# Optimization experiments

Measured on AMD Instinct MI355X. Metric: run time of the kernel, lower is better.

The kernel has to match this reference:

```python
import jax, jax.numpy as jnp
import numpy as np

ALPHA = 1.5
N_ITER = 5
N_SECTIONS = 5


def setup_inputs() -> dict:
    key = jax.random.key(0)
    X = jax.random.normal(key, (4096, 32000), dtype=jnp.float32)
    return {"X": X}


def reference(X) -> jnp.ndarray:
    # entmax_nsect: find tau such that sum_j [(alpha-1)*X_j - tau]_+^{1/(alpha-1)} = 1
    # via n-section search (n_iter rounds, interval split into n_sections).
    alpha = ALPHA
    Xs = X * (alpha - 1.0)                      # work in transformed logits
    d = X.shape[-1]
    exp_inv = 1.0 / (alpha - 1.0)

    max_val = jnp.max(Xs, axis=-1, keepdims=True)
    lo = max_val - 1.0                          # f(lo) >= 0
    hi = max_val - (1.0 / d) ** (alpha - 1.0)   # f(hi) <= 0

    def f(tau):
        # sum of p(tau) minus 1; monotonically decreasing in tau
        p = jnp.clip(Xs - tau, 0.0, None) ** exp_inv
        return jnp.sum(p, axis=-1, keepdims=True) - 1.0

    for _ in range(N_ITER):
        width = (hi - lo) / N_SECTIONS
        new_lo = lo
        # pick the largest interior grid point where f is still >= 0
        for k in range(1, N_SECTIONS):
            t = lo + k * width
            new_lo = jnp.where(f(t) >= 0.0, t, new_lo)
        lo = new_lo
        hi = new_lo + width

    tau = 0.5 * (lo + hi)
    p = jnp.clip(Xs - tau, 0.0, None) ** exp_inv
    # ensure_sum_one=True
    p = p / jnp.sum(p, axis=-1, keepdims=True)
    return p
```

## Files before the change

### kernel.cpp

```cpp
#include <hip/hip_runtime.h>
#include <math.h>

#define D_DIM 32000
#define NV4   8000
#define BLOCK 256
#define KMAX  32
#define NBINS 256

#define BINW_F   3.8844134767822285e-3f
#define INVBW_F  257.43893f

typedef float floatx4 __attribute__((ext_vector_type(4)));


__global__ void __launch_bounds__(BLOCK, 3)
entmax_nsect_kernel(const float* __restrict__ X, float* __restrict__ out, int n_rows) {
    const int row = blockIdx.x;
    if (row >= n_rows) return;
    const int tid  = threadIdx.x;
    const int lane = tid & 63;
    const int wid  = tid >> 6;

    __shared__ __align__(16) float sC[NBINS];
    __shared__ __align__(16) float sS[NBINS];
    __shared__ __align__(16) float sQ[NBINS];
    __shared__ float s_wmax[4];

    const float4* __restrict__ xrow = reinterpret_cast<const float4*>(X + (size_t)row * D_DIM);
    floatx4* __restrict__ orow      = reinterpret_cast<floatx4*>(out + (size_t)row * D_DIM);

    float4 v[KMAX];
#pragma unroll
    for (int k = 0; k < KMAX; ++k) {
        const int j = tid + k * BLOCK;
        if (j < NV4) v[k] = xrow[j];
        else         v[k] = make_float4(-INFINITY, -INFINITY, -INFINITY, -INFINITY);
    }
#pragma unroll
    for (int k = 0; k < KMAX; ++k)
        asm volatile("" : "+v"(v[k].x), "+v"(v[k].y), "+v"(v[k].z), "+v"(v[k].w));

    sC[tid] = 0.0f; sS[tid] = 0.0f; sQ[tid] = 0.0f;

    float mx = -INFINITY;
#pragma unroll
    for (int k = 0; k < KMAX; ++k)
        mx = fmaxf(mx, fmaxf(fmaxf(v[k].x, v[k].y), fmaxf(v[k].z, v[k].w)));
#pragma unroll
    for (int o = 32; o > 0; o >>= 1) mx = fmaxf(mx, __shfl_xor(mx, o));
    if (lane == 0) s_wmax[wid] = mx;
    __syncthreads();

    const float m0 = fmaxf(fmaxf(s_wmax[0], s_wmax[1]), fmaxf(s_wmax[2], s_wmax[3]));
    const float maxXs = 0.5f * m0;

#pragma unroll
    for (int k = 0; k < KMAX; ++k) {
        const float ys[4] = { fmaf(v[k].x, 0.5f, -maxXs),
                              fmaf(v[k].y, 0.5f, -maxXs),
                              fmaf(v[k].z, 0.5f, -maxXs),
                              fmaf(v[k].w, 0.5f, -maxXs) };
#pragma unroll
        for (int c = 0; c < 4; ++c) {
            const float y = ys[c];
            if (y > -1.0f) {
                const int b = (int)fminf((y + 1.0f) * INVBW_F, 255.0f);
                atomicAdd(&sC[b], 1.0f);
                atomicAdd(&sS[b], y);
                atomicAdd(&sQ[b], y * y);
            }
        }
    }
    __syncthreads();

    if (wid < 3) {
        float* plane = (wid == 0) ? sC : (wid == 1) ? sS : sQ;
        const float4 f = reinterpret_cast<const float4*>(plane)[lane];
        const float t3 = f.w;
        const float t2 = f.z + t3;
        const float t1 = f.y + t2;
        const float t0 = f.x + t1;
        float inc = t0;
#pragma unroll
        for (int o = 1; o < 64; o <<= 1) {
            const float u = __shfl_down(inc, o);
            if (lane + o < 64) inc += u;
        }
        const float above = inc - t0;
        float4 o4;
        o4.x = t0 + above; o4.y = t1 + above; o4.z = t2 + above; o4.w = t3 + above;
        reinterpret_cast<float4*>(plane)[lane] = o4;
    }
    __syncthreads();

    int klo = 0, khi = 256;
#pragma unroll
    for (int it = 0; it < 8; ++it) {
        const int mid = (klo + khi) >> 1;
        const float t  = fmaf((float)mid, BINW_F, -1.0f);
        const float fm = fmaf(t, fmaf(t, sC[mid], -2.0f * sS[mid]), sQ[mid]);
        if (fm >= 1.0f) klo = mid; else khi = mid;
    }
    const float C = sC[klo], S = sS[klo], Q = sQ[klo];
    const float disc = fmaxf(fmaf(S, S, -C * (Q - 1.0f)), 0.0f);
    float tauY = (S - sqrtf(disc)) / C;
    tauY = fminf(fmaxf(tauY, -1.0f), 0.0f);
    const float tau = maxXs + tauY;

#pragma unroll
    for (int k = 0; k < KMAX; ++k) {
        const int j = tid + k * BLOCK;
        if (j < NV4) {
            float d;
            floatx4 p;
            d = fmaxf(fmaf(v[k].x, 0.5f, -tau), 0.f); p.x = d * d;
            d = fmaxf(fmaf(v[k].y, 0.5f, -tau), 0.f); p.y = d * d;
            d = fmaxf(fmaf(v[k].z, 0.5f, -tau), 0.f); p.z = d * d;
            d = fmaxf(fmaf(v[k].w, 0.5f, -tau), 0.f); p.w = d * d;
            __builtin_nontemporal_store(p, &orow[j]);
        }
    }
}

extern "C" void kernel_launch(void* const* d_in, const int* in_sizes, int n_in,
                              void* d_out, int out_size, void* d_ws, size_t ws_size,
                              hipStream_t stream) {
    const float* X = (const float*)d_in[0];
    float* out     = (float*)d_out;
    const int n_rows = in_sizes[0] / D_DIM;
    entmax_nsect_kernel<<<dim3(n_rows), dim3(BLOCK), 0, stream>>>(X, out, n_rows);
}
```

Baseline: 204.4 us.

## Stream row from memory three times instead of caching it in registers

Drops the 32-float4 register cache of each row and re-reads the row from global memory in the max, histogram and output passes. The launch bound rises from 3 to 8 blocks per SIMD, so more waves can be resident to hide latency. Each row is 128KB, so re-reads are meant to hit L2 or the infinity cache. The trade-off is roughly three times more load traffic through the cache hierarchy, and a DRAM-bound slowdown if those re-reads miss.

```diff
diff --git a/kernel.cpp b/kernel.cpp
--- a/kernel.cpp
+++ b/kernel.cpp
@@ -4,7 +4,7 @@
 #define D_DIM 32000
 #define NV4   8000
 #define BLOCK 256
-#define KMAX  32
+#define KFULL 31
 #define NBINS 256
 
 #define BINW_F   3.8844134767822285e-3f
@@ -13,7 +13,7 @@
 typedef float floatx4 __attribute__((ext_vector_type(4)));
 
 
-__global__ void __launch_bounds__(BLOCK, 3)
+__global__ void __launch_bounds__(BLOCK, 8)
 entmax_nsect_kernel(const float* __restrict__ X, float* __restrict__ out, int n_rows) {
     const int row = blockIdx.x;
     if (row >= n_rows) return;
@@ -29,23 +29,18 @@
     const float4* __restrict__ xrow = reinterpret_cast<const float4*>(X + (size_t)row * D_DIM);
     floatx4* __restrict__ orow      = reinterpret_cast<floatx4*>(out + (size_t)row * D_DIM);
 
-    float4 v[KMAX];
-#pragma unroll
-    for (int k = 0; k < KMAX; ++k) {
-        const int j = tid + k * BLOCK;
-        if (j < NV4) v[k] = xrow[j];
-        else         v[k] = make_float4(-INFINITY, -INFINITY, -INFINITY, -INFINITY);
-    }
-#pragma unroll
-    for (int k = 0; k < KMAX; ++k)
-        asm volatile("" : "+v"(v[k].x), "+v"(v[k].y), "+v"(v[k].z), "+v"(v[k].w));
-
     sC[tid] = 0.0f; sS[tid] = 0.0f; sQ[tid] = 0.0f;
 
     float mx = -INFINITY;
-#pragma unroll
-    for (int k = 0; k < KMAX; ++k)
-        mx = fmaxf(mx, fmaxf(fmaxf(v[k].x, v[k].y), fmaxf(v[k].z, v[k].w)));
+#pragma unroll 4
+    for (int k = 0; k < KFULL; ++k) {
+        const float4 a = xrow[tid + k * BLOCK];
+        mx = fmaxf(mx, fmaxf(fmaxf(a.x, a.y), fmaxf(a.z, a.w)));
+    }
+    if (tid < 64) {
+        const float4 a = xrow[tid + KFULL * BLOCK];
+        mx = fmaxf(mx, fmaxf(fmaxf(a.x, a.y), fmaxf(a.z, a.w)));
+    }
 #pragma unroll
     for (int o = 32; o > 0; o >>= 1) mx = fmaxf(mx, __shfl_xor(mx, o));
     if (lane == 0) s_wmax[wid] = mx;
@@ -54,12 +49,26 @@
     const float m0 = fmaxf(fmaxf(s_wmax[0], s_wmax[1]), fmaxf(s_wmax[2], s_wmax[3]));
     const float maxXs = 0.5f * m0;
 
+#pragma unroll 4
+    for (int k = 0; k < KFULL; ++k) {
+        const float4 a = xrow[tid + k * BLOCK];
+        const float ys[4] = { fmaf(a.x, 0.5f, -maxXs), fmaf(a.y, 0.5f, -maxXs),
+                              fmaf(a.z, 0.5f, -maxXs), fmaf(a.w, 0.5f, -maxXs) };
 #pragma unroll
-    for (int k = 0; k < KMAX; ++k) {
-        const float ys[4] = { fmaf(v[k].x, 0.5f, -maxXs),
-                              fmaf(v[k].y, 0.5f, -maxXs),
-                              fmaf(v[k].z, 0.5f, -maxXs),
-                              fmaf(v[k].w, 0.5f, -maxXs) };
+        for (int c = 0; c < 4; ++c) {
+            const float y = ys[c];
+            if (y > -1.0f) {
+                const int b = (int)fminf((y + 1.0f) * INVBW_F, 255.0f);
+                atomicAdd(&sC[b], 1.0f);
+                atomicAdd(&sS[b], y);
+                atomicAdd(&sQ[b], y * y);
+            }
+        }
+    }
+    if (tid < 64) {
+        const float4 a = xrow[tid + KFULL * BLOCK];
+        const float ys[4] = { fmaf(a.x, 0.5f, -maxXs), fmaf(a.y, 0.5f, -maxXs),
+                              fmaf(a.z, 0.5f, -maxXs), fmaf(a.w, 0.5f, -maxXs) };
 #pragma unroll
         for (int c = 0; c < 4; ++c) {
             const float y = ys[c];
@@ -107,18 +116,26 @@
     tauY = fminf(fmaxf(tauY, -1.0f), 0.0f);
     const float tau = maxXs + tauY;
 
-#pragma unroll
-    for (int k = 0; k < KMAX; ++k) {
-        const int j = tid + k * BLOCK;
-        if (j < NV4) {
-            float d;
-            floatx4 p;
-            d = fmaxf(fmaf(v[k].x, 0.5f, -tau), 0.f); p.x = d * d;
-            d = fmaxf(fmaf(v[k].y, 0.5f, -tau), 0.f); p.y = d * d;
-            d = fmaxf(fmaf(v[k].z, 0.5f, -tau), 0.f); p.z = d * d;
-            d = fmaxf(fmaf(v[k].w, 0.5f, -tau), 0.f); p.w = d * d;
-            __builtin_nontemporal_store(p, &orow[j]);
-        }
+#pragma unroll 4
+    for (int k = 0; k < KFULL; ++k) {
+        const float4 a = xrow[tid + k * BLOCK];
+        float d;
+        floatx4 p;
+        d = fmaxf(fmaf(a.x, 0.5f, -tau), 0.f); p.x = d * d;
+        d = fmaxf(fmaf(a.y, 0.5f, -tau), 0.f); p.y = d * d;
+        d = fmaxf(fmaf(a.z, 0.5f, -tau), 0.f); p.z = d * d;
+        d = fmaxf(fmaf(a.w, 0.5f, -tau), 0.f); p.w = d * d;
+        __builtin_nontemporal_store(p, &orow[tid + k * BLOCK]);
+    }
+    if (tid < 64) {
+        const float4 a = xrow[tid + KFULL * BLOCK];
+        float d;
+        floatx4 p;
+        d = fmaxf(fmaf(a.x, 0.5f, -tau), 0.f); p.x = d * d;
+        d = fmaxf(fmaf(a.y, 0.5f, -tau), 0.f); p.y = d * d;
+        d = fmaxf(fmaf(a.z, 0.5f, -tau), 0.f); p.z = d * d;
+        d = fmaxf(fmaf(a.w, 0.5f, -tau), 0.f); p.w = d * d;
+        __builtin_nontemporal_store(p, &orow[tid + KFULL * BLOCK]);
     }
 }
 
```

New measurement: 285.1 us. +39.5%, slower.

## Process multiple rows per 1024-thread block with async LDS prefetch of next row

Applied to the files above, without the earlier changes.

Each block now handles 16 consecutive rows with 1024 threads. The next row is loaded straight from global memory into LDS through global_load_lds while the current row's histogram, scan and output phases run. The goal is to hide DRAM load latency behind compute and to cut per-block launch and setup overhead. The histogram shrinks to 224 bins with an adjusted bin width. The cost is a 128KB LDS buffer, which allows only one block per CU, so latency hiding rests on the single-buffer prefetch.

```diff
diff --git a/kernel.cpp b/kernel.cpp
--- a/kernel.cpp
+++ b/kernel.cpp
@@ -3,121 +3,163 @@
 
 #define D_DIM 32000
 #define NV4   8000
-#define BLOCK 256
-#define KMAX  32
-#define NBINS 256
+#define BLOCK 1024
+#define KREG  8
+#define RPB   16
+#define NBINS 224
 
-#define BINW_F   3.8844134767822285e-3f
-#define INVBW_F  257.43893f
+#define BINW_F   4.4393297e-3f
+#define INVBW_F  225.259277f
 
 typedef float floatx4 __attribute__((ext_vector_type(4)));
+typedef const __attribute__((address_space(1))) uint32_t kGlobU32;
+typedef __attribute__((address_space(3)))        uint32_t kLdsU32;
+
+__device__ __forceinline__ void gld_lds16(const float4* g, float4* l) {
+    __builtin_amdgcn_global_load_lds((kGlobU32*)g, (kLdsU32*)l, 16, 0, 0);
+}
+
+__device__ __forceinline__ void barrier_lds() {
+    asm volatile("s_waitcnt lgkmcnt(0)" ::: "memory");
+    __builtin_amdgcn_s_barrier();
+    asm volatile("" ::: "memory");
+}
+
+__device__ __forceinline__ void prefetch_row(const float4* __restrict__ xrow,
+                                             float4* sBuf, int wid, int lane) {
+    const int nch   = (wid == 15) ? 5 : 8;
+    const int base0 = wid * 512;
+#pragma unroll
+    for (int k = 0; k < 8; ++k) {
+        if (k < nch) {
+            const int base = base0 + (k << 6);
+            gld_lds16(xrow + base + lane, sBuf + base);
+        }
+    }
+}
 
 
-__global__ void __launch_bounds__(BLOCK, 3)
+__global__ void __launch_bounds__(BLOCK, 4)
 entmax_nsect_kernel(const float* __restrict__ X, float* __restrict__ out, int n_rows) {
-    const int row = blockIdx.x;
-    if (row >= n_rows) return;
     const int tid  = threadIdx.x;
     const int lane = tid & 63;
     const int wid  = tid >> 6;
+    const int row0 = blockIdx.x * RPB;
 
-    __shared__ __align__(16) float sC[NBINS];
-    __shared__ __align__(16) float sS[NBINS];
-    __shared__ __align__(16) float sQ[NBINS];
-    __shared__ float s_wmax[4];
+    __shared__ __align__(16) float4 sBuf[NV4 + 16];
+    __shared__ __align__(16) float  sC[NBINS];
+    __shared__ __align__(16) float  sS[NBINS];
+    __shared__ __align__(16) float  sQ[NBINS];
+    float* s_wmax = reinterpret_cast<float*>(&sBuf[NV4]);
 
-    const float4* __restrict__ xrow = reinterpret_cast<const float4*>(X + (size_t)row * D_DIM);
-    floatx4* __restrict__ orow      = reinterpret_cast<floatx4*>(out + (size_t)row * D_DIM);
+    if (row0 < n_rows)
+        prefetch_row(reinterpret_cast<const float4*>(X + (size_t)row0 * D_DIM), sBuf, wid, lane);
 
-    float4 v[KMAX];
+#pragma unroll 1
+    for (int i = 0; i < RPB; ++i) {
+        const int row = row0 + i;
+        if (row >= n_rows) break;
+
+        __syncthreads();
+
+        float4 v[KREG];
 #pragma unroll
-    for (int k = 0; k < KMAX; ++k) {
-        const int j = tid + k * BLOCK;
-        if (j < NV4) v[k] = xrow[j];
-        else         v[k] = make_float4(-INFINITY, -INFINITY, -INFINITY, -INFINITY);
-    }
+        for (int k = 0; k < KREG - 1; ++k) v[k] = sBuf[tid + k * BLOCK];
+        v[KREG - 1] = (tid < NV4 - (KREG - 1) * BLOCK)
+                          ? sBuf[tid + (KREG - 1) * BLOCK]
+                          : make_float4(-INFINITY, -INFINITY, -INFINITY, -INFINITY);
 #pragma unroll
-    for (int k = 0; k < KMAX; ++k)
-        asm volatile("" : "+v"(v[k].x), "+v"(v[k].y), "+v"(v[k].z), "+v"(v[k].w));
+        for (int k = 0; k < KREG; ++k)
+            asm volatile("" : "+v"(v[k].x), "+v"(v[k].y), "+v"(v[k].z), "+v"(v[k].w));
 
-    sC[tid] = 0.0f; sS[tid] = 0.0f; sQ[tid] = 0.0f;
+        if (tid < NBINS) { sC[tid] = 0.0f; sS[tid] = 0.0f; sQ[tid] = 0.0f; }
 
-    float mx = -INFINITY;
+        float mx = -INFINITY;
 #pragma unroll
-    for (int k = 0; k < KMAX; ++k)
-        mx = fmaxf(mx, fmaxf(fmaxf(v[k].x, v[k].y), fmaxf(v[k].z, v[k].w)));
+        for (int k = 0; k < KREG; ++k)
+            mx = fmaxf(mx, fmaxf(fmaxf(v[k].x, v[k].y), fmaxf(v[k].z, v[k].w)));
 #pragma unroll
-    for (int o = 32; o > 0; o >>= 1) mx = fmaxf(mx, __shfl_xor(mx, o));
-    if (lane == 0) s_wmax[wid] = mx;
-    __syncthreads();
+        for (int o = 32; o > 0; o >>= 1) mx = fmaxf(mx, __shfl_xor(mx, o));
+        if (lane == 0) s_wmax[wid] = mx;
 
-    const float m0 = fmaxf(fmaxf(s_wmax[0], s_wmax[1]), fmaxf(s_wmax[2], s_wmax[3]));
-    const float maxXs = 0.5f * m0;
+        __syncthreads();
+
+        if (row + 1 < n_rows && i + 1 < RPB)
+            prefetch_row(reinterpret_cast<const float4*>(X + (size_t)(row + 1) * D_DIM),
+                         sBuf, wid, lane);
+
+        float m0 = s_wmax[0];
+#pragma unroll
+        for (int w = 1; w < 16; ++w) m0 = fmaxf(m0, s_wmax[w]);
+        const float maxXs = 0.5f * m0;
 
 #pragma unroll
-    for (int k = 0; k < KMAX; ++k) {
-        const float ys[4] = { fmaf(v[k].x, 0.5f, -maxXs),
-                              fmaf(v[k].y, 0.5f, -maxXs),
-                              fmaf(v[k].z, 0.5f, -maxXs),
-                              fmaf(v[k].w, 0.5f, -maxXs) };
+        for (int k = 0; k < KREG; ++k) {
+            const float ys[4] = { fmaf(v[k].x, 0.5f, -maxXs), fmaf(v[k].y, 0.5f, -maxXs),
+                                  fmaf(v[k].z, 0.5f, -maxXs), fmaf(v[k].w, 0.5f, -maxXs) };
 #pragma unroll
-        for (int c = 0; c < 4; ++c) {
-            const float y = ys[c];
-            if (y > -1.0f) {
-                const int b = (int)fminf((y + 1.0f) * INVBW_F, 255.0f);
-                atomicAdd(&sC[b], 1.0f);
-                atomicAdd(&sS[b], y);
-                atomicAdd(&sQ[b], y * y);
+            for (int c = 0; c < 4; ++c) {
+                const float y = ys[c];
+                if (y > -1.0f) {
+                    const int b = (int)fminf((y + 1.0f) * INVBW_F, (float)(NBINS - 1));
+                    atomicAdd(&sC[b], 1.0f);
+                    atomicAdd(&sS[b], y);
+                    atomicAdd(&sQ[b], y * y);
+                }
             }
         }
-    }
-    __syncthreads();
+        barrier_lds();
 
-    if (wid < 3) {
-        float* plane = (wid == 0) ? sC : (wid == 1) ? sS : sQ;
-        const float4 f = reinterpret_cast<const float4*>(plane)[lane];
-        const float t3 = f.w;
-        const float t2 = f.z + t3;
-        const float t1 = f.y + t2;
-        const float t0 = f.x + t1;
-        float inc = t0;
+        if (wid < 3) {
+            float* plane = (wid == 0) ? sC : (wid == 1) ? sS : sQ;
+            float4 f = make_float4(0.f, 0.f, 0.f, 0.f);
+            if (lane < NBINS / 4) f = reinterpret_cast<const float4*>(plane)[lane];
+            const float t3 = f.w;
+            const float t2 = f.z + t3;
+            const float t1 = f.y + t2;
+            const float t0 = f.x + t1;
+            float inc = t0;
 #pragma unroll
-        for (int o = 1; o < 64; o <<= 1) {
-            const float u = __shfl_down(inc, o);
-            if (lane + o < 64) inc += u;
+            for (int o = 1; o < 64; o <<= 1) {
+                const float u = __shfl_down(inc, o);
+                if (lane + o < 64) inc += u;
+            }
+            const float above = inc - t0;
+            if (lane < NBINS / 4) {
+                float4 o4;
+                o4.x = t0 + above; o4.y = t1 + above; o4.z = t2 + above; o4.w = t3 + above;
+                reinterpret_cast<float4*>(plane)[lane] = o4;
+            }
         }
-        const float above = inc - t0;
-        float4 o4;
-        o4.x = t0 + above; o4.y = t1 + above; o4.z = t2 + above; o4.w = t3 + above;
-        reinterpret_cast<float4*>(plane)[lane] = o4;
-    }
-    __syncthreads();
+        barrier_lds();
 
-    int klo = 0, khi = 256;
+        int klo = 0, khi = NBINS;
 #pragma unroll
-    for (int it = 0; it < 8; ++it) {
-        const int mid = (klo + khi) >> 1;
-        const float t  = fmaf((float)mid, BINW_F, -1.0f);
-        const float fm = fmaf(t, fmaf(t, sC[mid], -2.0f * sS[mid]), sQ[mid]);
-        if (fm >= 1.0f) klo = mid; else khi = mid;
-    }
-    const float C = sC[klo], S = sS[klo], Q = sQ[klo];
-    const float disc = fmaxf(fmaf(S, S, -C * (Q - 1.0f)), 0.0f);
-    float tauY = (S - sqrtf(disc)) / C;
-    tauY = fminf(fmaxf(tauY, -1.0f), 0.0f);
-    const float tau = maxXs + tauY;
+        for (int it = 0; it < 8; ++it) {
+            const int mid = (klo + khi) >> 1;
+            const float t  = fmaf((float)mid, BINW_F, -1.0f);
+            const float fm = fmaf(t, fmaf(t, sC[mid], -2.0f * sS[mid]), sQ[mid]);
+            if (fm >= 1.0f) klo = mid; else khi = mid;
+        }
+        const float C = sC[klo], S = sS[klo], Q = sQ[klo];
+        const float disc = fmaxf(fmaf(S, S, -C * (Q - 1.0f)), 0.0f);
+        float tauY = (S - sqrtf(disc)) / C;
+        tauY = fminf(fmaxf(tauY, -1.0f), 0.0f);
+        const float tau = maxXs + tauY;
 
+        floatx4* __restrict__ orow = reinterpret_cast<floatx4*>(out + (size_t)row * D_DIM);
 #pragma unroll
-    for (int k = 0; k < KMAX; ++k) {
-        const int j = tid + k * BLOCK;
-        if (j < NV4) {
-            float d;
-            floatx4 p;
-            d = fmaxf(fmaf(v[k].x, 0.5f, -tau), 0.f); p.x = d * d;
-            d = fmaxf(fmaf(v[k].y, 0.5f, -tau), 0.f); p.y = d * d;
-            d = fmaxf(fmaf(v[k].z, 0.5f, -tau), 0.f); p.z = d * d;
-            d = fmaxf(fmaf(v[k].w, 0.5f, -tau), 0.f); p.w = d * d;
-            __builtin_nontemporal_store(p, &orow[j]);
+        for (int k = 0; k < KREG; ++k) {
+            const int j = tid + k * BLOCK;
+            if (j < NV4) {
+                float d;
+                floatx4 p;
+                d = fmaxf(fmaf(v[k].x, 0.5f, -tau), 0.f); p.x = d * d;
+                d = fmaxf(fmaf(v[k].y, 0.5f, -tau), 0.f); p.y = d * d;
+                d = fmaxf(fmaf(v[k].z, 0.5f, -tau), 0.f); p.z = d * d;
+                d = fmaxf(fmaf(v[k].w, 0.5f, -tau), 0.f); p.w = d * d;
+                __builtin_nontemporal_store(p, &orow[j]);
+            }
         }
     }
 }
@@ -128,5 +170,6 @@
     const float* X = (const float*)d_in[0];
     float* out     = (float*)d_out;
     const int n_rows = in_sizes[0] / D_DIM;
-    entmax_nsect_kernel<<<dim3(n_rows), dim3(BLOCK), 0, stream>>>(X, out, n_rows);
+    const int grid   = (n_rows + RPB - 1) / RPB;
+    entmax_nsect_kernel<<<dim3(grid), dim3(BLOCK), 0, stream>>>(X, out, n_rows);
 }
```

After: 207.9 us. No clear change (+1.7%).
